# Performance work log

Measured on AMD Instinct MI355X. Metric: run time of the kernel, lower is better.

The kernel has to match this reference:

```python
import jax, jax.numpy as jnp
import numpy as np

NEG = -1000000.0

def setup_inputs() -> dict:
    key = jax.random.key(0)
    ks = jax.random.split(key, 7)
    B, Lq, Lk, Dq, Dk, Dv, H = 4, 256, 1024, 512, 512, 512, 256
    return {
        "query": jax.random.normal(ks[0], (B, Lq, Dq), dtype=jnp.float32),
        "key": jax.random.normal(ks[1], (B, Lk, Dk), dtype=jnp.float32),
        "value": jax.random.normal(ks[2], (B, Lk, Dv), dtype=jnp.float32),
        "valid_len": jax.random.randint(ks[3], (B,), 1, Lk + 1),
        "Wq": jax.random.normal(ks[4], (Dq, H), dtype=jnp.float32) * (1.0 / np.sqrt(Dq)),
        "Wk": jax.random.normal(ks[5], (Dk, H), dtype=jnp.float32) * (1.0 / np.sqrt(Dk)),
        "wv": jax.random.normal(ks[6], (H,), dtype=jnp.float32) * (1.0 / np.sqrt(H)),
    }

def reference(query, key, value, valid_len, Wq, Wk, wv):
    # projections: [B,Lq,H], [B,Lk,H]
    q = jnp.einsum("bqd,dh->bqh", query, Wq)
    k = jnp.einsum("bkd,dh->bkh", key, Wk)
    # broadcast-add + tanh: [B,Lq,Lk,H]
    features = jnp.tanh(q[:, :, None, :] + k[:, None, :, :])
    # score projection to scalar: [B,Lq,Lk]
    score = jnp.einsum("bqkh,h->bqk", features, wv)
    # masked softmax over keys (valid_len per batch, broadcast over queries)
    Lk = key.shape[1]
    mask = jnp.arange(Lk)[None, None, :] < valid_len[:, None, None]
    score = jnp.where(mask, score, NEG)
    attn = jax.nn.softmax(score, axis=-1)
    # weighted sum of values: [B,Lq,Dv]  (dropout is identity in eval)
    return jnp.einsum("bqk,bkv->bqv", attn, value)
```

## Files before the change

kernel.cpp:

```cpp
#include <hip/hip_runtime.h>

typedef __attribute__((ext_vector_type(8))) short short8v;
typedef __attribute__((ext_vector_type(4))) float float4v;
typedef unsigned int uint;

#define TWO_LOG2E 2.8853900817779268f
#define LOG2E     1.4426950408889634f

__device__ inline uint rne_bf16(float x) {
    uint u = __float_as_uint(x);
    return (u + 0x7fffu + ((u >> 16) & 1u)) >> 16;
}
__device__ inline uint pack_hi_lo(float a0, float a1, uint& lo_pack) {
    const uint h0 = rne_bf16(a0), h1 = rne_bf16(a1);
    const float f0 = __uint_as_float(h0 << 16), f1 = __uint_as_float(h1 << 16);
    const float l0 = a0 - f0, l1 = a1 - f1;
    lo_pack = (rne_bf16(l1) << 16) | rne_bf16(l0);
    return (h1 << 16) | h0;
}
__device__ inline void split8(const float4 x0, const float4 x1,
                              short8v& h, short8v& l) {
    const float xs[8] = {x0.x, x0.y, x0.z, x0.w, x1.x, x1.y, x1.z, x1.w};
    #pragma unroll
    for (int j = 0; j < 8; ++j) {
        const uint u = __float_as_uint(xs[j]);
        const uint hi = u & 0xFFFF0000u;
        const float lo = xs[j] - __uint_as_float(hi);
        h[j] = (short)(hi >> 16);
        l[j] = (short)rne_bf16(lo);
    }
}

__global__ __launch_bounds__(256) void prep_w(
    const float* __restrict__ Wq, const float* __restrict__ Wk,
    ushort* __restrict__ WT_hi, ushort* __restrict__ WT_lo)
{
    const int t = blockIdx.x * 256 + threadIdx.x;
    const int n = t & 255;
    const int kg = ((t >> 8) & 63) * 8;
    const int w = t >> 14;
    const float* W = w ? Wk : Wq;
    float x[8];
    #pragma unroll
    for (int i = 0; i < 8; ++i) x[i] = W[(size_t)(kg + i) * 256 + n];
    uint h0, h1, h2, h3, l0, l1, l2, l3;
    h0 = pack_hi_lo(x[0], x[1], l0);
    h1 = pack_hi_lo(x[2], x[3], l1);
    h2 = pack_hi_lo(x[4], x[5], l2);
    h3 = pack_hi_lo(x[6], x[7], l3);
    const size_t off = ((size_t)w * 256 + n) * 512 + kg;
    *(uint4*)(WT_hi + off) = make_uint4(h0, h1, h2, h3);
    *(uint4*)(WT_lo + off) = make_uint4(l0, l1, l2, l3);
}

__global__ __launch_bounds__(256) void prep_v(
    const float* __restrict__ value, const int* __restrict__ vlen,
    ushort* __restrict__ VT_hi, ushort* __restrict__ VT_lo)
{
    __shared__ float t[64][69];
    const int b = blockIdx.z;
    const int k0 = blockIdx.y * 64, n0 = blockIdx.x * 64;
    const int kendB = (vlen[b] + 31) & ~31;
    if (k0 >= kendB) return;

    const int tid = threadIdx.x;
    const int n_in = (tid & 15) * 4, k_in = tid >> 4;
    const float* src = value + ((size_t)b * 1024 + k0 + k_in) * 512 + n0 + n_in;
    #pragma unroll
    for (int p = 0; p < 4; ++p) {
        const float4 x = *(const float4*)(src + (size_t)p * 16 * 512);
        t[k_in + p * 16][n_in + 0] = x.x;
        t[k_in + p * 16][n_in + 1] = x.y;
        t[k_in + p * 16][n_in + 2] = x.z;
        t[k_in + p * 16][n_in + 3] = x.w;
    }
    __syncthreads();

    const int rn = tid >> 2, c0 = (tid & 3) * 16;
    uint hp[8], lp[8];
    #pragma unroll
    for (int i = 0; i < 8; ++i)
        hp[i] = pack_hi_lo(t[c0 + 2 * i][rn], t[c0 + 2 * i + 1][rn], lp[i]);
    const size_t off = ((size_t)b * 512 + n0 + rn) * 1024 + k0 + c0;
    *(uint4*)(VT_hi + off) = make_uint4(hp[0], hp[1], hp[2], hp[3]);
    *(uint4*)(VT_hi + off + 8) = make_uint4(hp[4], hp[5], hp[6], hp[7]);
    *(uint4*)(VT_lo + off) = make_uint4(lp[0], lp[1], lp[2], lp[3]);
    *(uint4*)(VT_lo + off + 8) = make_uint4(lp[4], lp[5], lp[6], lp[7]);
}

#define LOADA(s, kbase) { const int ko = (kbase) + half * 8;                   \
    _Pragma("unroll") for (int f = 0; f < 2; ++f) {                            \
        const float4 x0 = *(const float4*)(a_f + (size_t)(f * 16) * 512 + ko); \
        const float4 x1 = *(const float4*)(a_f + (size_t)(f * 16) * 512 + ko + 4); \
        split8(x0, x1, ah##s[f], al##s[f]); } }

#define LOADB(s, kbase) { const int ko = (kbase) + half * 8;                   \
    _Pragma("unroll") for (int f = 0; f < 4; ++f) {                            \
        bh##s[f] = *(const short8v*)(wt_h + (size_t)(f * 16) * 512 + ko);      \
        bl##s[f] = *(const short8v*)(wt_l + (size_t)(f * 16) * 512 + ko); } }

#define MFMAS(s)                                                                          \
    _Pragma("unroll") for (int mf = 0; mf < 2; ++mf)                                      \
    _Pragma("unroll") for (int nf = 0; nf < 4; ++nf) {                                    \
        acc[mf][nf] = __builtin_amdgcn_mfma_f32_16x16x32_bf16(ah##s[mf], bh##s[nf], acc[mf][nf], 0, 0, 0); \
        acc[mf][nf] = __builtin_amdgcn_mfma_f32_16x16x32_bf16(ah##s[mf], bl##s[nf], acc[mf][nf], 0, 0, 0); \
        acc[mf][nf] = __builtin_amdgcn_mfma_f32_16x16x32_bf16(al##s[mf], bh##s[nf], acc[mf][nf], 0, 0, 0); }

__global__ __launch_bounds__(64) void proj_mfma(
    const float* __restrict__ query, const float* __restrict__ key,
    const ushort* __restrict__ WT_hi, const ushort* __restrict__ WT_lo,
    const int* __restrict__ valid_len,
    float* __restrict__ EqT, float* __restrict__ EkT)
{
    const int lane = threadIdx.x;
    const int n0 = blockIdx.x * 64;
    const int m0 = blockIdx.y * 32;
    const bool isq = (m0 < 1024);
    int b = 0, kk0 = 0;
    if (!isq) {
        kk0 = (m0 - 1024) & 1023;
        b = (m0 - 1024) >> 10;
        if (kk0 >= valid_len[b]) return;
    }
    const int r = lane & 15, half = lane >> 4;
    const size_t wsel = isq ? 0 : (size_t)256 * 512;
    const ushort* wt_h = WT_hi + wsel + (size_t)(n0 + r) * 512;
    const ushort* wt_l = WT_lo + wsel + (size_t)(n0 + r) * 512;
    const float* a_f = isq ? (query + (size_t)(m0 + r) * 512)
                           : (key + (size_t)(m0 - 1024 + r) * 512);

    float4v acc[2][4] = {{{0.f}}};
    short8v ah0[2], al0[2], bh0[4], bl0[4];
    short8v ah1[2], al1[2], bh1[4], bl1[4];

    LOADA(0, 0); LOADB(0, 0);
    for (int kt = 0; kt < 512; kt += 64) {
        LOADA(1, kt + 32); LOADB(1, kt + 32);
        MFMAS(0);
        if (kt + 64 < 512) { LOADA(0, kt + 64); LOADB(0, kt + 64); }
        MFMAS(1);
    }

    #pragma unroll
    for (int mf = 0; mf < 2; ++mf) {
        #pragma unroll
        for (int nf = 0; nf < 4; ++nf) {
            float4v e;
            #pragma unroll
            for (int i = 0; i < 4; ++i)
                e[i] = __builtin_amdgcn_exp2f(acc[mf][nf][i] * TWO_LOG2E);
            if (isq) {
                *(float4v*)(EqT + (size_t)(n0 + nf * 16 + r) * 1024 +
                            m0 + mf * 16 + half * 4) = e;
            } else {
                *(float4v*)(EkT + (size_t)(b * 256 + n0 + nf * 16 + r) * 1024 +
                            kk0 + mf * 16 + half * 4) = e;
            }
        }
    }
}

__global__ __launch_bounds__(1024) void score_partial(
    const float* __restrict__ EqT, const float* __restrict__ EkT,
    const float* __restrict__ wv, const int* __restrict__ valid_len,
    float* __restrict__ P)
{
    __shared__ float eqs[256][8];
    __shared__ float wvs[256];
    __shared__ float part[4][8][256];

    const int orig = blockIdx.x;
    const int wgid = (orig & 7) * 64 + (orig >> 3);
    const int qg = wgid & 31;
    const int rest = wgid >> 5;
    const int kt = rest & 3;
    const int b = rest >> 2;

    const int vlen = valid_len[b];
    if (kt * 256 >= vlen) return;

    const int tid = threadIdx.x;
    const int hq = tid >> 8, kl = tid & 255;
    const int k = kt * 256 + kl;
    const int q0 = qg * 8;

    if (tid < 256) wvs[tid] = wv[tid];
    {
        const int i0 = tid * 2;
        const int h = i0 >> 3, q = i0 & 7;
        const float* ep = EqT + (size_t)h * 1024 + b * 256 + q0 + q;
        eqs[h][q] = ep[0];
        eqs[h][q + 1] = ep[1];
    }
    __syncthreads();

    float acc[8] = {};
    if (k < vlen) {
        const float* ekp = EkT + (size_t)(b * 256 + hq * 64) * 1024 + k;
        #pragma unroll 2
        for (int h = 0; h < 64; ++h) {
            const float ek = ekp[(size_t)h * 1024];
            const float w = wvs[hq * 64 + h];
            const float4 e0 = *(const float4*)&eqs[hq * 64 + h][0];
            const float4 e1 = *(const float4*)&eqs[hq * 64 + h][4];
            acc[0] = fmaf(w, __builtin_amdgcn_rcpf(fmaf(e0.x, ek, 1.f)), acc[0]);
            acc[1] = fmaf(w, __builtin_amdgcn_rcpf(fmaf(e0.y, ek, 1.f)), acc[1]);
            acc[2] = fmaf(w, __builtin_amdgcn_rcpf(fmaf(e0.z, ek, 1.f)), acc[2]);
            acc[3] = fmaf(w, __builtin_amdgcn_rcpf(fmaf(e0.w, ek, 1.f)), acc[3]);
            acc[4] = fmaf(w, __builtin_amdgcn_rcpf(fmaf(e1.x, ek, 1.f)), acc[4]);
            acc[5] = fmaf(w, __builtin_amdgcn_rcpf(fmaf(e1.y, ek, 1.f)), acc[5]);
            acc[6] = fmaf(w, __builtin_amdgcn_rcpf(fmaf(e1.z, ek, 1.f)), acc[6]);
            acc[7] = fmaf(w, __builtin_amdgcn_rcpf(fmaf(e1.w, ek, 1.f)), acc[7]);
        }
    }

    #pragma unroll
    for (int q = 0; q < 8; ++q) part[hq][q][kl] = acc[q];
    __syncthreads();

    #pragma unroll
    for (int j = 0; j < 2; ++j) {
        const int q = hq * 2 + j;
        const float s = part[0][q][kl] + part[1][q][kl] +
                        part[2][q][kl] + part[3][q][kl];
        P[(size_t)(b * 256 + q0 + q) * 1024 + k] = -2.f * s;
    }
}

__global__ __launch_bounds__(1024) void softmax_kernel(
    const float* __restrict__ P, const int* __restrict__ valid_len,
    ushort* __restrict__ attn_hi, ushort* __restrict__ attn_lo)
{
    __shared__ float red[16][4];

    const int tid = threadIdx.x;
    const int b = blockIdx.x >> 6;
    const int q0 = (blockIdx.x & 63) << 2;

    const int vlen = valid_len[b];
    const int k = tid;
    const bool v = (k < vlen);

    float s[4], m[4];
    #pragma unroll
    for (int q = 0; q < 4; ++q) {
        s[q] = P[(size_t)(b * 256 + q0 + q) * 1024 + k];
        m[q] = v ? s[q] : -1e30f;
    }
    #pragma unroll
    for (int o = 32; o; o >>= 1) {
        #pragma unroll
        for (int q = 0; q < 4; ++q) m[q] = fmaxf(m[q], __shfl_xor(m[q], o));
    }
    const int wid = tid >> 6;
    if ((tid & 63) == 0) {
        #pragma unroll
        for (int q = 0; q < 4; ++q) red[wid][q] = m[q];
    }
    __syncthreads();
    #pragma unroll
    for (int q = 0; q < 4; ++q) {
        float mm = red[0][q];
        #pragma unroll
        for (int w = 1; w < 16; ++w) mm = fmaxf(mm, red[w][q]);
        m[q] = mm;
    }
    __syncthreads();

    float p[4], l[4];
    #pragma unroll
    for (int q = 0; q < 4; ++q) {
        p[q] = v ? __builtin_amdgcn_exp2f((s[q] - m[q]) * LOG2E) : 0.f;
        l[q] = p[q];
    }
    #pragma unroll
    for (int o = 32; o; o >>= 1) {
        #pragma unroll
        for (int q = 0; q < 4; ++q) l[q] += __shfl_xor(l[q], o);
    }
    if ((tid & 63) == 0) {
        #pragma unroll
        for (int q = 0; q < 4; ++q) red[wid][q] = l[q];
    }
    __syncthreads();
    #pragma unroll
    for (int q = 0; q < 4; ++q) {
        float ss = red[0][q];
        #pragma unroll
        for (int w = 1; w < 16; ++w) ss += red[w][q];
        const float a = p[q] * __builtin_amdgcn_rcpf(ss);
        const uint hi = rne_bf16(a);
        const float lo = a - __uint_as_float(hi << 16);
        const size_t off = (size_t)(b * 256 + q0 + q) * 1024 + k;
        attn_hi[off] = (ushort)hi;
        attn_lo[off] = (ushort)rne_bf16(lo);
    }
}

#define PVLOAD(s, ko) {                                   \
    ah##s = *(const short8v*)(ah_p + (ko));               \
    al##s = *(const short8v*)(al_p + (ko));               \
    bh0##s = *(const short8v*)(bh_p + (ko));              \
    bl0##s = *(const short8v*)(bl_p + (ko));              \
    bh1##s = *(const short8v*)(bh_p + 16 * 1024 + (ko));  \
    bl1##s = *(const short8v*)(bl_p + 16 * 1024 + (ko)); }

#define PVMFMA(s) {                                                              \
    acc0 = __builtin_amdgcn_mfma_f32_16x16x32_bf16(ah##s, bh0##s, acc0, 0, 0, 0); \
    acc0 = __builtin_amdgcn_mfma_f32_16x16x32_bf16(ah##s, bl0##s, acc0, 0, 0, 0); \
    acc0 = __builtin_amdgcn_mfma_f32_16x16x32_bf16(al##s, bh0##s, acc0, 0, 0, 0); \
    acc1 = __builtin_amdgcn_mfma_f32_16x16x32_bf16(ah##s, bh1##s, acc1, 0, 0, 0); \
    acc1 = __builtin_amdgcn_mfma_f32_16x16x32_bf16(ah##s, bl1##s, acc1, 0, 0, 0); \
    acc1 = __builtin_amdgcn_mfma_f32_16x16x32_bf16(al##s, bh1##s, acc1, 0, 0, 0); }

__global__ __launch_bounds__(256) void pv_mfma(
    const ushort* __restrict__ attn_hi, const ushort* __restrict__ attn_lo,
    const ushort* __restrict__ VT_hi, const ushort* __restrict__ VT_lo,
    const int* __restrict__ valid_len,
    float* __restrict__ out)
{
    const int orig = blockIdx.x;
    const int wgid = (orig & 7) * 32 + (orig >> 3);
    const int qb = wgid & 3;
    const int rest = wgid >> 2;
    const int b = rest & 3;
    const int nt = rest >> 2;

    const int wid = threadIdx.x >> 6, lane = threadIdx.x & 63;
    const int n0 = nt * 32;
    const int q0 = qb * 64 + wid * 16;
    const int r = lane & 15, half = lane >> 4;
    const int kend = (valid_len[b] + 31) & ~31;

    const ushort* ah_p = attn_hi + (size_t)(b * 256 + q0 + r) * 1024 + half * 8;
    const ushort* al_p = attn_lo + (size_t)(b * 256 + q0 + r) * 1024 + half * 8;
    const ushort* bh_p = VT_hi + (size_t)(b * 512 + n0 + r) * 1024 + half * 8;
    const ushort* bl_p = VT_lo + (size_t)(b * 512 + n0 + r) * 1024 + half * 8;

    float4v acc0 = {0.f}, acc1 = {0.f};
    short8v ah0, al0, bh00, bl00, bh10, bl10;
    short8v ah1, al1, bh01, bl01, bh11, bl11;

    PVLOAD(0, 0);
    for (int kt = 0; kt < kend; kt += 64) {
        if (kt + 32 < kend) PVLOAD(1, kt + 32);
        PVMFMA(0);
        if (kt + 64 < kend) PVLOAD(0, kt + 64);
        if (kt + 32 < kend) PVMFMA(1);
    }

    float* op = out + (size_t)b * 256 * 512 + (size_t)(q0 + half * 4) * 512 + n0 + r;
    #pragma unroll
    for (int i = 0; i < 4; ++i) {
        op[(size_t)i * 512] = acc0[i];
        op[(size_t)i * 512 + 16] = acc1[i];
    }
}

extern "C" void kernel_launch(void* const* d_in, const int* in_sizes, int n_in,
                              void* d_out, int out_size, void* d_ws, size_t ws_size,
                              hipStream_t stream)
{
    const float* query = (const float*)d_in[0];
    const float* key   = (const float*)d_in[1];
    const float* value = (const float*)d_in[2];
    const int*   vlen  = (const int*)d_in[3];
    const float* Wq    = (const float*)d_in[4];
    const float* Wk    = (const float*)d_in[5];
    const float* wv    = (const float*)d_in[6];
    float* out = (float*)d_out;

    float*  EqT     = (float*)d_ws;
    float*  EkT     = EqT + 262144;
    float*  P       = EkT + 1048576;
    ushort* WT_hi   = (ushort*)(P + 1048576);
    ushort* WT_lo   = WT_hi + 262144;
    ushort* attn_hi = WT_lo + 262144;
    ushort* attn_lo = attn_hi + 1048576;
    ushort* VT_hi   = attn_lo + 1048576;
    ushort* VT_lo   = VT_hi + 2097152;

    hipLaunchKernelGGL(prep_w, dim3(128), dim3(256), 0, stream,
                       Wq, Wk, WT_hi, WT_lo);
    hipLaunchKernelGGL(prep_v, dim3(8, 16, 4), dim3(256), 0, stream,
                       value, vlen, VT_hi, VT_lo);
    hipLaunchKernelGGL(proj_mfma, dim3(4, 160), dim3(64), 0, stream,
                       query, key, WT_hi, WT_lo, vlen, EqT, EkT);
    hipLaunchKernelGGL(score_partial, dim3(512), dim3(1024), 0, stream,
                       EqT, EkT, wv, vlen, P);
    hipLaunchKernelGGL(softmax_kernel, dim3(256), dim3(1024), 0, stream,
                       P, vlen, attn_hi, attn_lo);
    hipLaunchKernelGGL(pv_mfma, dim3(256), dim3(256), 0, stream,
                       attn_hi, attn_lo, VT_hi, VT_lo, vlen, out);
}
```

Before: 86.02 us.

## Register-tile score kernel 4x4 and split H into partial score buffers

Restructures the score kernel so each thread computes a 4-query by 4-key register tile over one quarter of the hidden dimension, with vectorized float4 loads of Ek and Eq. The shared-memory cross-quarter reduction is removed. Each H-quarter now writes its own partial score plane, and the softmax kernel sums the four planes and applies the -2 scale. This raises reuse per loaded element and drops a sync and shared-memory round trip, at the cost of four times the P workspace and extra global reads in softmax.

```diff
diff --git a/kernel.cpp b/kernel.cpp
--- a/kernel.cpp
+++ b/kernel.cpp
@@ -160,70 +160,66 @@
     }
 }
 
-__global__ __launch_bounds__(1024) void score_partial(
+__global__ __launch_bounds__(256) void score_partial(
     const float* __restrict__ EqT, const float* __restrict__ EkT,
     const float* __restrict__ wv, const int* __restrict__ valid_len,
     float* __restrict__ P)
 {
-    __shared__ float eqs[256][8];
-    __shared__ float wvs[256];
-    __shared__ float part[4][8][256];
+    __shared__ float eqs[64][16];
+    __shared__ float wvs[64];
 
     const int orig = blockIdx.x;
-    const int wgid = (orig & 7) * 64 + (orig >> 3);
-    const int qg = wgid & 31;
-    const int rest = wgid >> 5;
-    const int kt = rest & 3;
-    const int b = rest >> 2;
+    const int wgid = (orig & 7) * 128 + (orig >> 3);
+    const int qt = wgid & 15;
+    const int kt = (wgid >> 4) & 3;
+    const int hq = (wgid >> 6) & 3;
+    const int b  = wgid >> 8;
 
     const int vlen = valid_len[b];
     if (kt * 256 >= vlen) return;
 
     const int tid = threadIdx.x;
-    const int hq = tid >> 8, kl = tid & 255;
-    const int k = kt * 256 + kl;
-    const int q0 = qg * 8;
-
-    if (tid < 256) wvs[tid] = wv[tid];
+    const int kg = tid & 63, qg = tid >> 6;
+    const int k0 = kt * 256 + kg * 4;
+    const int q0 = qt * 16;
+    const int h0 = hq * 64;
+
+    if (tid < 64) wvs[tid] = wv[h0 + tid];
     {
-        const int i0 = tid * 2;
-        const int h = i0 >> 3, q = i0 & 7;
-        const float* ep = EqT + (size_t)h * 1024 + b * 256 + q0 + q;
-        eqs[h][q] = ep[0];
-        eqs[h][q + 1] = ep[1];
-    }
-    __syncthreads();
-
-    float acc[8] = {};
-    if (k < vlen) {
-        const float* ekp = EkT + (size_t)(b * 256 + hq * 64) * 1024 + k;
+        const int i = tid * 4;
+        const int h = i >> 4, q = i & 15;
+        *(float4*)&eqs[h][q] =
+            *(const float4*)(EqT + (size_t)(h0 + h) * 1024 + b * 256 + q0 + q);
+    }
+    __syncthreads();
+
+    float acc[4][4] = {};
+    if (k0 < vlen) {
+        const float* ekp = EkT + (size_t)(b * 256 + h0) * 1024 + k0;
         #pragma unroll 2
         for (int h = 0; h < 64; ++h) {
-            const float ek = ekp[(size_t)h * 1024];
-            const float w = wvs[hq * 64 + h];
-            const float4 e0 = *(const float4*)&eqs[hq * 64 + h][0];
-            const float4 e1 = *(const float4*)&eqs[hq * 64 + h][4];
-            acc[0] = fmaf(w, __builtin_amdgcn_rcpf(fmaf(e0.x, ek, 1.f)), acc[0]);
-            acc[1] = fmaf(w, __builtin_amdgcn_rcpf(fmaf(e0.y, ek, 1.f)), acc[1]);
-            acc[2] = fmaf(w, __builtin_amdgcn_rcpf(fmaf(e0.z, ek, 1.f)), acc[2]);
-            acc[3] = fmaf(w, __builtin_amdgcn_rcpf(fmaf(e0.w, ek, 1.f)), acc[3]);
-            acc[4] = fmaf(w, __builtin_amdgcn_rcpf(fmaf(e1.x, ek, 1.f)), acc[4]);
-            acc[5] = fmaf(w, __builtin_amdgcn_rcpf(fmaf(e1.y, ek, 1.f)), acc[5]);
-            acc[6] = fmaf(w, __builtin_amdgcn_rcpf(fmaf(e1.z, ek, 1.f)), acc[6]);
-            acc[7] = fmaf(w, __builtin_amdgcn_rcpf(fmaf(e1.w, ek, 1.f)), acc[7]);
+            const float4 ek = *(const float4*)(ekp + (size_t)h * 1024);
+            const float4 eq = *(const float4*)&eqs[h][qg * 4];
+            const float w = wvs[h];
+            const float ekv[4] = {ek.x, ek.y, ek.z, ek.w};
+            const float eqv[4] = {eq.x, eq.y, eq.z, eq.w};
+            #pragma unroll
+            for (int qi = 0; qi < 4; ++qi) {
+                const float e = eqv[qi];
+                acc[qi][0] = fmaf(w, __builtin_amdgcn_rcpf(fmaf(e, ekv[0], 1.f)), acc[qi][0]);
+                acc[qi][1] = fmaf(w, __builtin_amdgcn_rcpf(fmaf(e, ekv[1], 1.f)), acc[qi][1]);
+                acc[qi][2] = fmaf(w, __builtin_amdgcn_rcpf(fmaf(e, ekv[2], 1.f)), acc[qi][2]);
+                acc[qi][3] = fmaf(w, __builtin_amdgcn_rcpf(fmaf(e, ekv[3], 1.f)), acc[qi][3]);
+            }
         }
     }
 
-    #pragma unroll
-    for (int q = 0; q < 8; ++q) part[hq][q][kl] = acc[q];
-    __syncthreads();
-
-    #pragma unroll
-    for (int j = 0; j < 2; ++j) {
-        const int q = hq * 2 + j;
-        const float s = part[0][q][kl] + part[1][q][kl] +
-                        part[2][q][kl] + part[3][q][kl];
-        P[(size_t)(b * 256 + q0 + q) * 1024 + k] = -2.f * s;
+    float* Pq = P + (size_t)hq * (1024 * 1024);
+    #pragma unroll
+    for (int qi = 0; qi < 4; ++qi) {
+        float4 o;
+        o.x = acc[qi][0]; o.y = acc[qi][1]; o.z = acc[qi][2]; o.w = acc[qi][3];
+        *(float4*)(Pq + (size_t)(b * 256 + q0 + qg * 4 + qi) * 1024 + k0) = o;
     }
 }
 
@@ -244,7 +240,9 @@
     float s[4], m[4];
     #pragma unroll
     for (int q = 0; q < 4; ++q) {
-        s[q] = P[(size_t)(b * 256 + q0 + q) * 1024 + k];
+        const size_t off = (size_t)(b * 256 + q0 + q) * 1024 + k;
+        s[q] = -2.f * (P[off] + P[off + 1048576] +
+                       P[off + 2097152] + P[off + 3145728]);
         m[q] = v ? s[q] : -1e30f;
     }
     #pragma unroll
@@ -373,7 +371,7 @@
     float*  EqT     = (float*)d_ws;
     float*  EkT     = EqT + 262144;
     float*  P       = EkT + 1048576;
-    ushort* WT_hi   = (ushort*)(P + 1048576);
+    ushort* WT_hi   = (ushort*)(P + 4194304);
     ushort* WT_lo   = WT_hi + 262144;
     ushort* attn_hi = WT_lo + 262144;
     ushort* attn_lo = attn_hi + 1048576;
@@ -386,7 +384,7 @@
                        value, vlen, VT_hi, VT_lo);
     hipLaunchKernelGGL(proj_mfma, dim3(4, 160), dim3(64), 0, stream,
                        query, key, WT_hi, WT_lo, vlen, EqT, EkT);
-    hipLaunchKernelGGL(score_partial, dim3(512), dim3(1024), 0, stream,
+    hipLaunchKernelGGL(score_partial, dim3(1024), dim3(256), 0, stream,
                        EqT, EkT, wv, vlen, P);
     hipLaunchKernelGGL(softmax_kernel, dim3(256), dim3(1024), 0, stream,
                        P, vlen, attn_hi, attn_lo);
```

Result: slower. 93.02 us (+8.1%).
